# Optimization experiments

Hardware: AMD Instinct MI355X
Metric: run time of the kernel (lower is better)

## Reference

```python
import jax, jax.numpy as jnp
import numpy as np

N = 50000      # nodes
E = 800000     # edges
CIN = 128
CH = 128
COUT = 64
EPS = 1e-5     # BatchNorm eps


def setup_inputs() -> dict:
    key = jax.random.key(0)
    ks = jax.random.split(key, 16)
    s = 0.1  # weight scale for numerical stability
    return {
        "x": jax.random.normal(ks[0], (N, CIN), jnp.float32),
        "edge_index": jax.random.randint(ks[1], (2, E), 0, N, jnp.int32),
        "edge_weights": jax.random.uniform(ks[2], (E,), jnp.float32),
        "w1": jax.random.normal(ks[3], (CIN, CH), jnp.float32) * s,
        "b1": jnp.zeros((CH,), jnp.float32),
        "bn1_g": jnp.ones((CH,), jnp.float32),
        "bn1_b": jnp.zeros((CH,), jnp.float32),
        "bn1_m": jax.random.normal(ks[4], (CH,), jnp.float32) * 0.1,
        "bn1_v": jax.random.uniform(ks[5], (CH,), jnp.float32) + 0.5,
        "conv_ws": jax.random.normal(ks[6], (2, CH, CH), jnp.float32) * s,
        "conv_bs": jnp.zeros((2, CH), jnp.float32),
        "bns_g": jnp.ones((2, CH), jnp.float32),
        "bns_b": jnp.zeros((2, CH), jnp.float32),
        "bns_m": jax.random.normal(ks[7], (2, CH), jnp.float32) * 0.1,
        "bns_v": jax.random.uniform(ks[8], (2, CH), jnp.float32) + 0.5,
        "lin1_w": jax.random.normal(ks[9], (CH, CH), jnp.float32) * s,
        "lin1_b": jnp.zeros((CH,), jnp.float32),
        "lin2_w": jax.random.normal(ks[10], (CH, COUT), jnp.float32) * s,
        "lin2_b": jnp.zeros((COUT,), jnp.float32),
    }


def _bn(h, g, b, m, v):
    # BatchNorm1d in eval mode: running statistics
    return (h - m) * jax.lax.rsqrt(v + EPS) * g + b


def _gcn(h, w, b, src, dst, norm, n):
    # GCNConv: out[dst] += norm_e * (h @ W)[src]  (self loops already in src/dst)
    h = h @ w
    msg = h[src] * norm[:, None]                 # [E+N, CH]
    return jax.ops.segment_sum(msg, dst, num_segments=n) + b


def reference(x, edge_index, edge_weights, w1, b1, bn1_g, bn1_b, bn1_m, bn1_v,
              conv_ws, conv_bs, bns_g, bns_b, bns_m, bns_v,
              lin1_w, lin1_b, lin2_w, lin2_b):
    n = x.shape[0]
    loop = jnp.arange(n, dtype=edge_index.dtype)
    src = jnp.concatenate([edge_index[0], loop])
    dst = jnp.concatenate([edge_index[1], loop])
    ew = jnp.concatenate([edge_weights, jnp.ones((n,), edge_weights.dtype)])
    # symmetric degree normalization (PyG gcn_norm)
    deg = jax.ops.segment_sum(ew, dst, num_segments=n)
    dis = jnp.where(deg > 0, jax.lax.rsqrt(deg), 0.0)
    norm = dis[src] * ew * dis[dst]

    lrelu = jax.nn.leaky_relu  # slope 0.01, matches F.leaky_relu default
    h = lrelu(_bn(_gcn(x, w1, b1, src, dst, norm, n), bn1_g, bn1_b, bn1_m, bn1_v))
    for i in range(conv_ws.shape[0]):
        h = lrelu(_bn(_gcn(h, conv_ws[i], conv_bs[i], src, dst, norm, n),
                      bns_g[i], bns_b[i], bns_m[i], bns_v[i]) + h)
    h = lrelu(h @ lin1_w + lin1_b)
    # dropout is identity in eval mode
    return h @ lin2_w + lin2_b
```

## Files before the change

kernel.cpp:

```cpp
#include <hip/hip_runtime.h>
#include <hip/hip_bf16.h>


constexpr int   NN    = 50000;
constexpr int   EE    = 800000;
constexpr int   CH    = 128;
constexpr int   SLOTS = 64;
constexpr int   NBUK  = 782;
constexpr int   RCAP  = 2048;
constexpr int   EPB   = 4096;
constexpr float EPS   = 1e-5f;

typedef __attribute__((ext_vector_type(8))) short bf16x8;
typedef __attribute__((ext_vector_type(4))) float f32x4;
typedef unsigned long long u64;
typedef unsigned short u16;

__device__ inline u16 f2bf_rne(float f) {
  unsigned u = __float_as_uint(f);
  unsigned r = u + 0x7fffu + ((u >> 16) & 1u);
  return (u16)(r >> 16);
}
__device__ inline float bf2f(unsigned h16) {
  return __uint_as_float(h16 << 16);
}


__global__ __launch_bounds__(256) void bin_kernel(const int* __restrict__ ei,
                                                  const float* __restrict__ ew,
                                                  unsigned* __restrict__ gcur,
                                                  u64* __restrict__ bins) {
  __shared__ unsigned cnt[NBUK];
  __shared__ unsigned base[NBUK];
  const int tid = threadIdx.x;
  for (int b = tid; b < NBUK; b += 256) cnt[b] = 0;
  __syncthreads();
  const int e0 = blockIdx.x * EPB;
  unsigned pk[16]; u16 bkt[16]; u16 rnk[16]; unsigned char dl[16];
  #pragma unroll
  for (int i = 0; i < 16; i++) {
    int e = e0 + i * 256 + tid;
    if (e < EE) {
      int s = ei[e], d = ei[EE + e];
      float w = ew[e];
      bkt[i] = (u16)(d >> 6);
      dl[i]  = (unsigned char)(d & 63);
      pk[i]  = ((unsigned)f2bf_rne(w) << 16) | (unsigned)s;
      rnk[i] = (u16)atomicAdd(&cnt[bkt[i]], 1u);
    } else bkt[i] = 0xffffu;
  }
  __syncthreads();
  for (int b = tid; b < NBUK; b += 256) {
    unsigned c = cnt[b];
    base[b] = c ? atomicAdd(&gcur[b * 16], c) : 0u;
  }
  __syncthreads();
  #pragma unroll
  for (int i = 0; i < 16; i++) {
    if (bkt[i] == 0xffffu) continue;
    unsigned pos = base[bkt[i]] + rnk[i];
    if (pos < RCAP)
      bins[(size_t)bkt[i] * RCAP + pos] = ((u64)dl[i] << 32) | pk[i];
  }
}


__global__ __launch_bounds__(256) void scatter_kernel(const unsigned* __restrict__ gcur,
                                                      const u64* __restrict__ bins,
                                                      unsigned* __restrict__ ell,
                                                      float* __restrict__ dis) {
  __shared__ unsigned rank[64];
  __shared__ float    wsum[64];
  const int b   = blockIdx.x;
  const int tid = threadIdx.x;
  if (tid < 64) { rank[tid] = 1u; wsum[tid] = 0.f; }
  __syncthreads();
  unsigned cnt = gcur[b * 16];
  if (cnt > RCAP) cnt = RCAP;
  const u64* src = bins + (size_t)b * RCAP;
  for (unsigned i = tid; i < cnt; i += 256) {
    u64 v = src[i];
    unsigned pk = (unsigned)v;
    unsigned dl = (unsigned)(v >> 32);
    unsigned r = atomicAdd(&rank[dl], 1u);
    if (r < SLOTS)
      ell[((size_t)(b * 64 + dl)) * SLOTS + r] = pk;
    atomicAdd(&wsum[dl], bf2f(pk >> 16));
  }
  __syncthreads();
  if (tid < 64) {
    int node = b * 64 + tid;
    if (node < NN) {
      unsigned c = rank[tid];
      if (c > SLOTS) c = SLOTS;
      ell[(size_t)node * SLOTS] = c;
      dis[node] = rsqrtf(1.0f + wsum[tid]);
    }
  }
}

constexpr int NB_WZ = (73728 + 384 + 255) / 256;

__global__ void wswz_kernel(
    const float* __restrict__ w1, const float* __restrict__ bn1_g, const float* __restrict__ bn1_v,
    const float* __restrict__ conv_ws, const float* __restrict__ bns_g, const float* __restrict__ bns_v,
    const float* __restrict__ lin1_w, const float* __restrict__ lin2_w,
    const float* __restrict__ b1, const float* __restrict__ bn1_b, const float* __restrict__ bn1_m,
    const float* __restrict__ conv_bs, const float* __restrict__ bns_b, const float* __restrict__ bns_m,
    u16* __restrict__ w1h, u16* __restrict__ w1l,
    u16* __restrict__ c0h, u16* __restrict__ c0l,
    u16* __restrict__ c1h, u16* __restrict__ c1l,
    u16* __restrict__ l1h, u16* __restrict__ l1l,
    u16* __restrict__ l2h, u16* __restrict__ l2l,
    float* __restrict__ beff)
{
  int idx = blockIdx.x * 256 + threadIdx.x;
  if (idx >= 73728) {
    int r = idx - 73728;
    if (r >= 384) return;
    int l = r >> 7, c = r & 127;
    float bc, gg, bb, mm, vv;
    if (l == 0) { bc = b1[c]; gg = bn1_g[c]; bb = bn1_b[c]; mm = bn1_m[c]; vv = bn1_v[c]; }
    else {
      int o = (l - 1) * 128 + c;
      bc = conv_bs[o]; gg = bns_g[o]; bb = bns_b[o]; mm = bns_m[o]; vv = bns_v[o];
    }
    beff[r] = (bc - mm) * gg * rsqrtf(vv + EPS) + bb;
    return;
  }
  const float* W; const float* g = nullptr; const float* v = nullptr;
  u16 *hi, *lo; int CO = 128; int local;
  if      (idx < 16384) { W = w1;              g = bn1_g;     v = bn1_v;     hi = w1h; lo = w1l; local = idx; }
  else if (idx < 32768) { W = conv_ws;         g = bns_g;     v = bns_v;     hi = c0h; lo = c0l; local = idx - 16384; }
  else if (idx < 49152) { W = conv_ws + 16384; g = bns_g+128; v = bns_v+128; hi = c1h; lo = c1l; local = idx - 32768; }
  else if (idx < 65536) { W = lin1_w;                                        hi = l1h; lo = l1l; local = idx - 49152; }
  else                  { W = lin2_w;                                        hi = l2h; lo = l2l; local = idx - 65536; CO = 64; }
  int k = local / CO, n = local % CO;
  float w = W[local];
  if (g) w *= g[n] * rsqrtf(v[n] + EPS);
  int NCT = CO / 16;
  int kchunk = k >> 5, kin = k & 31, quad = kin >> 3, j = kin & 7;
  int ct = n >> 4, l = (quad << 4) | (n & 15);
  size_t pos = ((size_t)(kchunk * NCT + ct) * 64 + l) * 8 + j;
  u16 h = f2bf_rne(w);
  hi[pos] = h;
  lo[pos] = f2bf_rne(w - bf2f(h));
}

__global__ __launch_bounds__(256) void gemm1_kernel(
    const float* __restrict__ Ain,
    const u16* __restrict__ Whi, const u16* __restrict__ Wlo,
    const float* __restrict__ dis, u16* __restrict__ Cout)
{
  __shared__ float lds[64][CH + 4];
  const int tid  = threadIdx.x;
  const int wave = tid >> 6;
  const int lane = tid & 63;
  const int quad = lane >> 4;
  const int mrow = lane & 15;
  const int row0 = blockIdx.x * 64;

  int arow = row0 + wave * 16 + mrow;
  if (arow >= NN) arow = NN - 1;

  bf16x8 ahi[4], alo[4];
  const float* Ar = Ain + (size_t)arow * CH;
  #pragma unroll
  for (int c = 0; c < 4; c++) {
    int off = c * 32 + quad * 8;
    float4 f0 = *(const float4*)(Ar + off);
    float4 f1 = *(const float4*)(Ar + off + 4);
    float f[8] = {f0.x, f0.y, f0.z, f0.w, f1.x, f1.y, f1.z, f1.w};
    #pragma unroll
    for (int j = 0; j < 8; j++) {
      u16 h = f2bf_rne(f[j]);
      ahi[c][j] = (short)h;
      alo[c][j] = (short)f2bf_rne(f[j] - bf2f(h));
    }
  }

  f32x4 acc[8];
  #pragma unroll
  for (int t = 0; t < 8; t++) acc[t] = (f32x4){0.f, 0.f, 0.f, 0.f};
  #pragma unroll
  for (int c = 0; c < 4; c++) {
    #pragma unroll
    for (int t = 0; t < 8; t++) {
      size_t base = ((size_t)(c * 8 + t) * 64 + lane) * 8;
      bf16x8 bh = *(const bf16x8*)(Whi + base);
      bf16x8 bl = *(const bf16x8*)(Wlo + base);
      acc[t] = __builtin_amdgcn_mfma_f32_16x16x32_bf16(ahi[c], bh, acc[t], 0, 0, 0);
      acc[t] = __builtin_amdgcn_mfma_f32_16x16x32_bf16(alo[c], bh, acc[t], 0, 0, 0);
      acc[t] = __builtin_amdgcn_mfma_f32_16x16x32_bf16(ahi[c], bl, acc[t], 0, 0, 0);
    }
  }

  #pragma unroll
  for (int t = 0; t < 8; t++)
    #pragma unroll
    for (int r = 0; r < 4; r++)
      lds[wave * 16 + quad * 4 + r][t * 16 + mrow] = acc[t][r];
  __syncthreads();

  #pragma unroll
  for (int i = tid; i < 64 * CH / 4; i += 256) {
    int row = (i * 4) / CH;
    int col = (i * 4) % CH;
    int grow = row0 + row;
    if (grow >= NN) continue;
    float rs = dis[grow];
    const float* lp = &lds[row][col];
    u16* cp = (u16*)Cout + (size_t)grow * CH + col;
    unsigned p0 = ((unsigned)f2bf_rne(lp[1] * rs) << 16) | f2bf_rne(lp[0] * rs);
    unsigned p1 = ((unsigned)f2bf_rne(lp[3] * rs) << 16) | f2bf_rne(lp[2] * rs);
    *(uint2*)cp = make_uint2(p0, p1);
  }
}

template<bool RES>
__global__ __launch_bounds__(256, 5) void fuse_kernel(
    const u16* __restrict__ hwin,
    const unsigned* __restrict__ ell, const float* __restrict__ dis,
    const float* __restrict__ beff, const u16* __restrict__ res,
    const u16* __restrict__ Whi, const u16* __restrict__ Wlo,
    u16* __restrict__ hout, u16* __restrict__ hwout)
{
  __shared__ unsigned hs[64][68];
  const int tid  = threadIdx.x;
  const int wave = tid >> 6;
  const int lane = tid & 63;
  const int sub  = lane & 15;
  const int grp  = lane >> 4;
  const int row0 = blockIdx.x * 64;

  for (int r = 0; r < 16; r++) {
    int node = row0 + wave * 16 + r;
    int nd = node < NN ? node : NN - 1;
    unsigned myword = ell[(size_t)nd * SLOTS + lane];
    int cnt = __shfl((int)myword, 0);
    if (cnt > SLOTS) cnt = SLOTS;
    float a[8] = {0.f, 0.f, 0.f, 0.f, 0.f, 0.f, 0.f, 0.f};
    for (int j = 0; j < cnt; j += 16) {
      unsigned sidx[4]; float wv[4];
      #pragma unroll
      for (int q = 0; q < 4; q++) {
        int jj = j + q * 4 + grp;
        unsigned e = (unsigned)__shfl((int)myword, jj & 63);
        float    w = (jj == 0) ? 1.0f : bf2f(e >> 16);
        unsigned s = (jj == 0) ? (unsigned)nd : (e & 0xffffu);
        if (jj >= cnt) { w = 0.f; s = (unsigned)nd; }
        sidx[q] = s; wv[q] = w;
      }
      uint4 h[4];
      #pragma unroll
      for (int q = 0; q < 4; q++)
        h[q] = *(const uint4*)(hwin + (size_t)sidx[q] * CH + sub * 8);
      #pragma unroll
      for (int q = 0; q < 4; q++) {
        float w = wv[q];
        a[0] = fmaf(w, bf2f(h[q].x & 0xffffu), a[0]); a[1] = fmaf(w, bf2f(h[q].x >> 16), a[1]);
        a[2] = fmaf(w, bf2f(h[q].y & 0xffffu), a[2]); a[3] = fmaf(w, bf2f(h[q].y >> 16), a[3]);
        a[4] = fmaf(w, bf2f(h[q].z & 0xffffu), a[4]); a[5] = fmaf(w, bf2f(h[q].z >> 16), a[5]);
        a[6] = fmaf(w, bf2f(h[q].w & 0xffffu), a[6]); a[7] = fmaf(w, bf2f(h[q].w >> 16), a[7]);
      }
    }
    #pragma unroll
    for (int k = 0; k < 8; k++) {
      a[k] += __shfl_xor(a[k], 16);
      a[k] += __shfl_xor(a[k], 32);
    }
    if (grp == 0) {
      float disd = dis[nd];
      int c = sub * 8;
      float4 be0 = *(const float4*)(beff + c);
      float4 be1 = *(const float4*)(beff + c + 4);
      float y[8];
      y[0] = a[0] * disd + be0.x; y[1] = a[1] * disd + be0.y;
      y[2] = a[2] * disd + be0.z; y[3] = a[3] * disd + be0.w;
      y[4] = a[4] * disd + be1.x; y[5] = a[5] * disd + be1.y;
      y[6] = a[6] * disd + be1.z; y[7] = a[7] * disd + be1.w;
      if constexpr (RES) {
        uint4 rr = *(const uint4*)(res + (size_t)nd * CH + c);
        y[0] += bf2f(rr.x & 0xffffu); y[1] += bf2f(rr.x >> 16);
        y[2] += bf2f(rr.y & 0xffffu); y[3] += bf2f(rr.y >> 16);
        y[4] += bf2f(rr.z & 0xffffu); y[5] += bf2f(rr.z >> 16);
        y[6] += bf2f(rr.w & 0xffffu); y[7] += bf2f(rr.w >> 16);
      }
      #pragma unroll
      for (int k = 0; k < 8; k++) y[k] = y[k] > 0.f ? y[k] : 0.01f * y[k];
      uint4 o;
      o.x = ((unsigned)f2bf_rne(y[1]) << 16) | f2bf_rne(y[0]);
      o.y = ((unsigned)f2bf_rne(y[3]) << 16) | f2bf_rne(y[2]);
      o.z = ((unsigned)f2bf_rne(y[5]) << 16) | f2bf_rne(y[4]);
      o.w = ((unsigned)f2bf_rne(y[7]) << 16) | f2bf_rne(y[6]);
      if (node < NN) *(uint4*)(hout + (size_t)node * CH + c) = o;
      *(uint4*)&hs[wave * 16 + r][sub * 4] = o;
    }
  }

  bf16x8 af[4];
  #pragma unroll
  for (int c = 0; c < 4; c++)
    af[c] = *(const bf16x8*)&hs[wave * 16 + sub][c * 16 + grp * 4];

  f32x4 acc[8];
  #pragma unroll
  for (int t = 0; t < 8; t++) acc[t] = (f32x4){0.f, 0.f, 0.f, 0.f};
  #pragma unroll
  for (int c = 0; c < 4; c++) {
    #pragma unroll
    for (int t = 0; t < 8; t++) {
      size_t base = ((size_t)(c * 8 + t) * 64 + lane) * 8;
      bf16x8 bh = *(const bf16x8*)(Whi + base);
      bf16x8 bl = *(const bf16x8*)(Wlo + base);
      acc[t] = __builtin_amdgcn_mfma_f32_16x16x32_bf16(af[c], bh, acc[t], 0, 0, 0);
      acc[t] = __builtin_amdgcn_mfma_f32_16x16x32_bf16(af[c], bl, acc[t], 0, 0, 0);
    }
  }

  #pragma unroll
  for (int r = 0; r < 4; r++) {
    int grow = row0 + wave * 16 + grp * 4 + r;
    if (grow >= NN) continue;
    float rs = dis[grow];
    #pragma unroll
    for (int t = 0; t < 8; t++)
      hwout[(size_t)grow * CH + t * 16 + sub] = f2bf_rne(acc[t][r] * rs);
  }
}

__global__ __launch_bounds__(256, 4) void fuse_last_kernel(
    const u16* __restrict__ hwin,
    const unsigned* __restrict__ ell, const float* __restrict__ dis,
    const float* __restrict__ beff, const u16* __restrict__ res,
    const u16* __restrict__ l1h, const u16* __restrict__ l1l,
    const float* __restrict__ b1,
    const u16* __restrict__ l2h, const u16* __restrict__ l2l,
    const float* __restrict__ b2, float* __restrict__ out)
{
  __shared__ unsigned smem[64 * 132];
  float* fs = (float*)smem;
  const int tid  = threadIdx.x;
  const int wave = tid >> 6;
  const int lane = tid & 63;
  const int sub  = lane & 15;
  const int grp  = lane >> 4;
  const int row0 = blockIdx.x * 64;

  for (int r = 0; r < 16; r++) {
    int node = row0 + wave * 16 + r;
    int nd = node < NN ? node : NN - 1;
    unsigned myword = ell[(size_t)nd * SLOTS + lane];
    int cnt = __shfl((int)myword, 0);
    if (cnt > SLOTS) cnt = SLOTS;
    float a[8] = {0.f, 0.f, 0.f, 0.f, 0.f, 0.f, 0.f, 0.f};
    for (int j = 0; j < cnt; j += 16) {
      unsigned sidx[4]; float wv[4];
      #pragma unroll
      for (int q = 0; q < 4; q++) {
        int jj = j + q * 4 + grp;
        unsigned e = (unsigned)__shfl((int)myword, jj & 63);
        float    w = (jj == 0) ? 1.0f : bf2f(e >> 16);
        unsigned s = (jj == 0) ? (unsigned)nd : (e & 0xffffu);
        if (jj >= cnt) { w = 0.f; s = (unsigned)nd; }
        sidx[q] = s; wv[q] = w;
      }
      uint4 h[4];
      #pragma unroll
      for (int q = 0; q < 4; q++)
        h[q] = *(const uint4*)(hwin + (size_t)sidx[q] * CH + sub * 8);
      #pragma unroll
      for (int q = 0; q < 4; q++) {
        float w = wv[q];
        a[0] = fmaf(w, bf2f(h[q].x & 0xffffu), a[0]); a[1] = fmaf(w, bf2f(h[q].x >> 16), a[1]);
        a[2] = fmaf(w, bf2f(h[q].y & 0xffffu), a[2]); a[3] = fmaf(w, bf2f(h[q].y >> 16), a[3]);
        a[4] = fmaf(w, bf2f(h[q].z & 0xffffu), a[4]); a[5] = fmaf(w, bf2f(h[q].z >> 16), a[5]);
        a[6] = fmaf(w, bf2f(h[q].w & 0xffffu), a[6]); a[7] = fmaf(w, bf2f(h[q].w >> 16), a[7]);
      }
    }
    #pragma unroll
    for (int k = 0; k < 8; k++) {
      a[k] += __shfl_xor(a[k], 16);
      a[k] += __shfl_xor(a[k], 32);
    }
    if (grp == 0) {
      float disd = dis[nd];
      int c = sub * 8;
      float4 be0 = *(const float4*)(beff + c);
      float4 be1 = *(const float4*)(beff + c + 4);
      float y[8];
      y[0] = a[0] * disd + be0.x; y[1] = a[1] * disd + be0.y;
      y[2] = a[2] * disd + be0.z; y[3] = a[3] * disd + be0.w;
      y[4] = a[4] * disd + be1.x; y[5] = a[5] * disd + be1.y;
      y[6] = a[6] * disd + be1.z; y[7] = a[7] * disd + be1.w;
      uint4 rr = *(const uint4*)(res + (size_t)nd * CH + c);
      y[0] += bf2f(rr.x & 0xffffu); y[1] += bf2f(rr.x >> 16);
      y[2] += bf2f(rr.y & 0xffffu); y[3] += bf2f(rr.y >> 16);
      y[4] += bf2f(rr.z & 0xffffu); y[5] += bf2f(rr.z >> 16);
      y[6] += bf2f(rr.w & 0xffffu); y[7] += bf2f(rr.w >> 16);
      #pragma unroll
      for (int k = 0; k < 8; k++) y[k] = y[k] > 0.f ? y[k] : 0.01f * y[k];
      uint4 o;
      o.x = ((unsigned)f2bf_rne(y[1]) << 16) | f2bf_rne(y[0]);
      o.y = ((unsigned)f2bf_rne(y[3]) << 16) | f2bf_rne(y[2]);
      o.z = ((unsigned)f2bf_rne(y[5]) << 16) | f2bf_rne(y[4]);
      o.w = ((unsigned)f2bf_rne(y[7]) << 16) | f2bf_rne(y[6]);
      *(uint4*)&smem[(wave * 16 + r) * 68 + sub * 4] = o;
    }
  }

  bf16x8 af[4];
  #pragma unroll
  for (int c = 0; c < 4; c++)
    af[c] = *(const bf16x8*)&smem[(wave * 16 + sub) * 68 + c * 16 + grp * 4];
  __syncthreads();

  f32x4 acc[8];
  #pragma unroll
  for (int t = 0; t < 8; t++) acc[t] = (f32x4){0.f, 0.f, 0.f, 0.f};
  #pragma unroll
  for (int c = 0; c < 4; c++) {
    #pragma unroll
    for (int t = 0; t < 8; t++) {
      size_t base = ((size_t)(c * 8 + t) * 64 + lane) * 8;
      bf16x8 bh = *(const bf16x8*)(l1h + base);
      bf16x8 bl = *(const bf16x8*)(l1l + base);
      acc[t] = __builtin_amdgcn_mfma_f32_16x16x32_bf16(af[c], bh, acc[t], 0, 0, 0);
      acc[t] = __builtin_amdgcn_mfma_f32_16x16x32_bf16(af[c], bl, acc[t], 0, 0, 0);
    }
  }
  #pragma unroll
  for (int t = 0; t < 8; t++) {
    float bb = b1[t * 16 + sub];
    #pragma unroll
    for (int r = 0; r < 4; r++) {
      float x = acc[t][r] + bb;
      x = x > 0.f ? x : 0.01f * x;
      fs[(wave * 16 + grp * 4 + r) * 132 + t * 16 + sub] = x;
    }
  }

  f32x4 acc2[4];
  #pragma unroll
  for (int t = 0; t < 4; t++) acc2[t] = (f32x4){0.f, 0.f, 0.f, 0.f};
  #pragma unroll
  for (int c = 0; c < 4; c++) {
    bf16x8 ahi, alo;
    const float* lp = &fs[(wave * 16 + sub) * 132 + c * 32 + grp * 8];
    float4 f0 = *(const float4*)lp;
    float4 f1 = *(const float4*)(lp + 4);
    float f[8] = {f0.x, f0.y, f0.z, f0.w, f1.x, f1.y, f1.z, f1.w};
    #pragma unroll
    for (int j = 0; j < 8; j++) {
      u16 h = f2bf_rne(f[j]);
      ahi[j] = (short)h;
      alo[j] = (short)f2bf_rne(f[j] - bf2f(h));
    }
    #pragma unroll
    for (int t = 0; t < 4; t++) {
      size_t base = ((size_t)(c * 4 + t) * 64 + lane) * 8;
      bf16x8 bh = *(const bf16x8*)(l2h + base);
      bf16x8 bl = *(const bf16x8*)(l2l + base);
      acc2[t] = __builtin_amdgcn_mfma_f32_16x16x32_bf16(ahi, bh, acc2[t], 0, 0, 0);
      acc2[t] = __builtin_amdgcn_mfma_f32_16x16x32_bf16(alo, bh, acc2[t], 0, 0, 0);
      acc2[t] = __builtin_amdgcn_mfma_f32_16x16x32_bf16(ahi, bl, acc2[t], 0, 0, 0);
    }
  }
  #pragma unroll
  for (int t = 0; t < 4; t++) {
    float bb = b2[t * 16 + sub];
    #pragma unroll
    for (int r = 0; r < 4; r++) {
      int grow = row0 + wave * 16 + grp * 4 + r;
      if (grow < NN)
        out[(size_t)grow * 64 + t * 16 + sub] = acc2[t][r] + bb;
    }
  }
}


extern "C" void kernel_launch(void* const* d_in, const int* in_sizes, int n_in,
                              void* d_out, int out_size, void* d_ws, size_t ws_size,
                              hipStream_t stream) {
  const float* x       = (const float*)d_in[0];
  const int*   ei      = (const int*)  d_in[1];
  const float* ew      = (const float*)d_in[2];
  const float* w1      = (const float*)d_in[3];
  const float* b1      = (const float*)d_in[4];
  const float* bn1_g   = (const float*)d_in[5];
  const float* bn1_b   = (const float*)d_in[6];
  const float* bn1_m   = (const float*)d_in[7];
  const float* bn1_v   = (const float*)d_in[8];
  const float* conv_ws = (const float*)d_in[9];
  const float* conv_bs = (const float*)d_in[10];
  const float* bns_g   = (const float*)d_in[11];
  const float* bns_b   = (const float*)d_in[12];
  const float* bns_m   = (const float*)d_in[13];
  const float* bns_v   = (const float*)d_in[14];
  const float* lin1_w  = (const float*)d_in[15];
  const float* lin1_b  = (const float*)d_in[16];
  const float* lin2_w  = (const float*)d_in[17];
  const float* lin2_b  = (const float*)d_in[18];
  float* out = (float*)d_out;

  size_t off = 0;
  auto alloc = [&](size_t elems) -> void* {
    void* p = (char*)d_ws + off * 4;
    off += (elems + 3) & ~(size_t)3;
    return p;
  };
  unsigned* gcur = (unsigned*)alloc(NBUK * 16);
  u64*      bins = (u64*)     alloc((size_t)NBUK * RCAP * 2);
  unsigned* ell  = (unsigned*)alloc((size_t)NN * SLOTS);
  float*    dis  = (float*)   alloc(NN);
  float*    beff = (float*)   alloc(3 * CH);
  u16*      hwa  = (u16*)     alloc((size_t)NN * CH / 2);
  u16*      hwb  = (u16*)     alloc((size_t)NN * CH / 2);
  u16*      h1   = (u16*)     alloc((size_t)NN * CH / 2);
  u16*      h2   = (u16*)     alloc((size_t)NN * CH / 2);
  u16* w1h = (u16*)alloc(CH * CH / 2); u16* w1l = (u16*)alloc(CH * CH / 2);
  u16* c0h = (u16*)alloc(CH * CH / 2); u16* c0l = (u16*)alloc(CH * CH / 2);
  u16* c1h = (u16*)alloc(CH * CH / 2); u16* c1l = (u16*)alloc(CH * CH / 2);
  u16* l1h = (u16*)alloc(CH * CH / 2); u16* l1l = (u16*)alloc(CH * CH / 2);
  u16* l2h = (u16*)alloc(CH * 64 / 2); u16* l2l = (u16*)alloc(CH * 64 / 2);

  const int nb_bin  = (EE + EPB - 1) / EPB;
  const int nb_gemm = (NN + 63) / 64;
  dim3 B(256);

  hipMemsetAsync(gcur, 0, NBUK * 16 * sizeof(unsigned), stream);
  bin_kernel    <<<nb_bin, B, 0, stream>>>(ei, ew, gcur, bins);
  scatter_kernel<<<NBUK,   B, 0, stream>>>(gcur, bins, ell, dis);

  wswz_kernel<<<NB_WZ, B, 0, stream>>>(w1, bn1_g, bn1_v, conv_ws, bns_g, bns_v,
      lin1_w, lin2_w, b1, bn1_b, bn1_m, conv_bs, bns_b, bns_m,
      w1h, w1l, c0h, c0l, c1h, c1l, l1h, l1l, l2h, l2l, beff);

  gemm1_kernel<<<nb_gemm, B, 0, stream>>>(x, w1h, w1l, dis, hwa);

  fuse_kernel<false><<<nb_gemm, B, 0, stream>>>(hwa, ell, dis, beff, nullptr,
      c0h, c0l, h1, hwb);

  fuse_kernel<true><<<nb_gemm, B, 0, stream>>>(hwb, ell, dis, beff + CH, h1,
      c1h, c1l, h2, hwa);

  fuse_last_kernel<<<nb_gemm, B, 0, stream>>>(hwa, ell, dis, beff + 2 * CH, h2,
      l1h, l1l, lin1_b, l2h, l2l, lin2_b, out);
}
```

Measured before the change: 313.8 us.

## Shrink fused GCN blocks to 16 nodes and split GEMM columns across waves

The fused aggregate+GEMM kernels now process 16 nodes per block instead of 64. Each wave gathers 4 nodes, and the ELL row for the next node is prefetched one step ahead. The block then synchronises and each wave computes a 32-column slice (or 16 for the last layer) of the 16-row MFMA GEMM. This launches about four times as many blocks and raises the occupancy hint, aiming to improve load balance and latency hiding in the gather. The cost is an added block barrier and each block re-reading the weights for only 16 rows.

```diff
diff --git a/kernel.cpp b/kernel.cpp
--- a/kernel.cpp
+++ b/kernel.cpp
@@ -218,99 +218,109 @@
 }
 
 template<bool RES>
-__global__ __launch_bounds__(256, 5) void fuse_kernel(
+__global__ __launch_bounds__(256, 6) void fuse_kernel(
     const u16* __restrict__ hwin,
     const unsigned* __restrict__ ell, const float* __restrict__ dis,
     const float* __restrict__ beff, const u16* __restrict__ res,
     const u16* __restrict__ Whi, const u16* __restrict__ Wlo,
     u16* __restrict__ hout, u16* __restrict__ hwout)
 {
-  __shared__ unsigned hs[64][68];
+  __shared__ unsigned hs[16][68];
   const int tid  = threadIdx.x;
   const int wave = tid >> 6;
   const int lane = tid & 63;
   const int sub  = lane & 15;
   const int grp  = lane >> 4;
-  const int row0 = blockIdx.x * 64;
-
-  for (int r = 0; r < 16; r++) {
-    int node = row0 + wave * 16 + r;
-    int nd = node < NN ? node : NN - 1;
-    unsigned myword = ell[(size_t)nd * SLOTS + lane];
-    int cnt = __shfl((int)myword, 0);
-    if (cnt > SLOTS) cnt = SLOTS;
-    float a[8] = {0.f, 0.f, 0.f, 0.f, 0.f, 0.f, 0.f, 0.f};
-    for (int j = 0; j < cnt; j += 16) {
-      unsigned sidx[4]; float wv[4];
+  const int row0 = blockIdx.x * 16;
+
+  const int nbase = row0 + wave * 4;
+  {
+    int nd0 = nbase < NN ? nbase : NN - 1;
+    unsigned wcur = ell[(size_t)nd0 * SLOTS + lane];
+    for (int r = 0; r < 4; r++) {
+      int node = nbase + r;
+      int nd = node < NN ? node : NN - 1;
+      unsigned myword = wcur;
+      if (r < 3) {
+        int n2 = node + 1 < NN ? node + 1 : NN - 1;
+        wcur = ell[(size_t)n2 * SLOTS + lane];
+      }
+      int cnt = __shfl((int)myword, 0);
+      if (cnt > SLOTS) cnt = SLOTS;
+      float a[8] = {0.f, 0.f, 0.f, 0.f, 0.f, 0.f, 0.f, 0.f};
+      for (int j = 0; j < cnt; j += 16) {
+        unsigned sidx[4]; float wv[4];
+        #pragma unroll
+        for (int q = 0; q < 4; q++) {
+          int jj = j + q * 4 + grp;
+          unsigned e = (unsigned)__shfl((int)myword, jj & 63);
+          float    w = (jj == 0) ? 1.0f : bf2f(e >> 16);
+          unsigned s = (jj == 0) ? (unsigned)nd : (e & 0xffffu);
+          if (jj >= cnt) { w = 0.f; s = (unsigned)nd; }
+          sidx[q] = s; wv[q] = w;
+        }
+        uint4 h[4];
+        #pragma unroll
+        for (int q = 0; q < 4; q++)
+          h[q] = *(const uint4*)(hwin + (size_t)sidx[q] * CH + sub * 8);
+        #pragma unroll
+        for (int q = 0; q < 4; q++) {
+          float w = wv[q];
+          a[0] = fmaf(w, bf2f(h[q].x & 0xffffu), a[0]); a[1] = fmaf(w, bf2f(h[q].x >> 16), a[1]);
+          a[2] = fmaf(w, bf2f(h[q].y & 0xffffu), a[2]); a[3] = fmaf(w, bf2f(h[q].y >> 16), a[3]);
+          a[4] = fmaf(w, bf2f(h[q].z & 0xffffu), a[4]); a[5] = fmaf(w, bf2f(h[q].z >> 16), a[5]);
+          a[6] = fmaf(w, bf2f(h[q].w & 0xffffu), a[6]); a[7] = fmaf(w, bf2f(h[q].w >> 16), a[7]);
+        }
+      }
       #pragma unroll
-      for (int q = 0; q < 4; q++) {
-        int jj = j + q * 4 + grp;
-        unsigned e = (unsigned)__shfl((int)myword, jj & 63);
-        float    w = (jj == 0) ? 1.0f : bf2f(e >> 16);
-        unsigned s = (jj == 0) ? (unsigned)nd : (e & 0xffffu);
-        if (jj >= cnt) { w = 0.f; s = (unsigned)nd; }
-        sidx[q] = s; wv[q] = w;
-      }
-      uint4 h[4];
-      #pragma unroll
-      for (int q = 0; q < 4; q++)
-        h[q] = *(const uint4*)(hwin + (size_t)sidx[q] * CH + sub * 8);
-      #pragma unroll
-      for (int q = 0; q < 4; q++) {
-        float w = wv[q];
-        a[0] = fmaf(w, bf2f(h[q].x & 0xffffu), a[0]); a[1] = fmaf(w, bf2f(h[q].x >> 16), a[1]);
-        a[2] = fmaf(w, bf2f(h[q].y & 0xffffu), a[2]); a[3] = fmaf(w, bf2f(h[q].y >> 16), a[3]);
-        a[4] = fmaf(w, bf2f(h[q].z & 0xffffu), a[4]); a[5] = fmaf(w, bf2f(h[q].z >> 16), a[5]);
-        a[6] = fmaf(w, bf2f(h[q].w & 0xffffu), a[6]); a[7] = fmaf(w, bf2f(h[q].w >> 16), a[7]);
-      }
-    }
-    #pragma unroll
-    for (int k = 0; k < 8; k++) {
-      a[k] += __shfl_xor(a[k], 16);
-      a[k] += __shfl_xor(a[k], 32);
-    }
-    if (grp == 0) {
-      float disd = dis[nd];
-      int c = sub * 8;
-      float4 be0 = *(const float4*)(beff + c);
-      float4 be1 = *(const float4*)(beff + c + 4);
-      float y[8];
-      y[0] = a[0] * disd + be0.x; y[1] = a[1] * disd + be0.y;
-      y[2] = a[2] * disd + be0.z; y[3] = a[3] * disd + be0.w;
-      y[4] = a[4] * disd + be1.x; y[5] = a[5] * disd + be1.y;
-      y[6] = a[6] * disd + be1.z; y[7] = a[7] * disd + be1.w;
-      if constexpr (RES) {
-        uint4 rr = *(const uint4*)(res + (size_t)nd * CH + c);
-        y[0] += bf2f(rr.x & 0xffffu); y[1] += bf2f(rr.x >> 16);
-        y[2] += bf2f(rr.y & 0xffffu); y[3] += bf2f(rr.y >> 16);
-        y[4] += bf2f(rr.z & 0xffffu); y[5] += bf2f(rr.z >> 16);
-        y[6] += bf2f(rr.w & 0xffffu); y[7] += bf2f(rr.w >> 16);
-      }
-      #pragma unroll
-      for (int k = 0; k < 8; k++) y[k] = y[k] > 0.f ? y[k] : 0.01f * y[k];
-      uint4 o;
-      o.x = ((unsigned)f2bf_rne(y[1]) << 16) | f2bf_rne(y[0]);
-      o.y = ((unsigned)f2bf_rne(y[3]) << 16) | f2bf_rne(y[2]);
-      o.z = ((unsigned)f2bf_rne(y[5]) << 16) | f2bf_rne(y[4]);
-      o.w = ((unsigned)f2bf_rne(y[7]) << 16) | f2bf_rne(y[6]);
-      if (node < NN) *(uint4*)(hout + (size_t)node * CH + c) = o;
-      *(uint4*)&hs[wave * 16 + r][sub * 4] = o;
-    }
-  }
+      for (int k = 0; k < 8; k++) {
+        a[k] += __shfl_xor(a[k], 16);
+        a[k] += __shfl_xor(a[k], 32);
+      }
+      if (grp == 0) {
+        float disd = dis[nd];
+        int c = sub * 8;
+        float4 be0 = *(const float4*)(beff + c);
+        float4 be1 = *(const float4*)(beff + c + 4);
+        float y[8];
+        y[0] = a[0] * disd + be0.x; y[1] = a[1] * disd + be0.y;
+        y[2] = a[2] * disd + be0.z; y[3] = a[3] * disd + be0.w;
+        y[4] = a[4] * disd + be1.x; y[5] = a[5] * disd + be1.y;
+        y[6] = a[6] * disd + be1.z; y[7] = a[7] * disd + be1.w;
+        if constexpr (RES) {
+          uint4 rr = *(const uint4*)(res + (size_t)nd * CH + c);
+          y[0] += bf2f(rr.x & 0xffffu); y[1] += bf2f(rr.x >> 16);
+          y[2] += bf2f(rr.y & 0xffffu); y[3] += bf2f(rr.y >> 16);
+          y[4] += bf2f(rr.z & 0xffffu); y[5] += bf2f(rr.z >> 16);
+          y[6] += bf2f(rr.w & 0xffffu); y[7] += bf2f(rr.w >> 16);
+        }
+        #pragma unroll
+        for (int k = 0; k < 8; k++) y[k] = y[k] > 0.f ? y[k] : 0.01f * y[k];
+        uint4 o;
+        o.x = ((unsigned)f2bf_rne(y[1]) << 16) | f2bf_rne(y[0]);
+        o.y = ((unsigned)f2bf_rne(y[3]) << 16) | f2bf_rne(y[2]);
+        o.z = ((unsigned)f2bf_rne(y[5]) << 16) | f2bf_rne(y[4]);
+        o.w = ((unsigned)f2bf_rne(y[7]) << 16) | f2bf_rne(y[6]);
+        if (node < NN) *(uint4*)(hout + (size_t)node * CH + c) = o;
+        *(uint4*)&hs[wave * 4 + r][sub * 4] = o;
+      }
+    }
+  }
+  __syncthreads();
 
   bf16x8 af[4];
   #pragma unroll
   for (int c = 0; c < 4; c++)
-    af[c] = *(const bf16x8*)&hs[wave * 16 + sub][c * 16 + grp * 4];
-
-  f32x4 acc[8];
-  #pragma unroll
-  for (int t = 0; t < 8; t++) acc[t] = (f32x4){0.f, 0.f, 0.f, 0.f};
+    af[c] = *(const bf16x8*)&hs[sub][c * 16 + grp * 4];
+
+  f32x4 acc[2];
+  #pragma unroll
+  for (int t = 0; t < 2; t++) acc[t] = (f32x4){0.f, 0.f, 0.f, 0.f};
   #pragma unroll
   for (int c = 0; c < 4; c++) {
     #pragma unroll
-    for (int t = 0; t < 8; t++) {
-      size_t base = ((size_t)(c * 8 + t) * 64 + lane) * 8;
+    for (int t = 0; t < 2; t++) {
+      size_t base = ((size_t)(c * 8 + wave * 2 + t) * 64 + lane) * 8;
       bf16x8 bh = *(const bf16x8*)(Whi + base);
       bf16x8 bl = *(const bf16x8*)(Wlo + base);
       acc[t] = __builtin_amdgcn_mfma_f32_16x16x32_bf16(af[c], bh, acc[t], 0, 0, 0);
@@ -320,16 +330,16 @@
 
   #pragma unroll
   for (int r = 0; r < 4; r++) {
-    int grow = row0 + wave * 16 + grp * 4 + r;
+    int grow = row0 + grp * 4 + r;
     if (grow >= NN) continue;
     float rs = dis[grow];
     #pragma unroll
-    for (int t = 0; t < 8; t++)
-      hwout[(size_t)grow * CH + t * 16 + sub] = f2bf_rne(acc[t][r] * rs);
-  }
-}
-
-__global__ __launch_bounds__(256, 4) void fuse_last_kernel(
+    for (int t = 0; t < 2; t++)
+      hwout[(size_t)grow * CH + wave * 32 + t * 16 + sub] = f2bf_rne(acc[t][r] * rs);
+  }
+}
+
+__global__ __launch_bounds__(256, 6) void fuse_last_kernel(
     const u16* __restrict__ hwin,
     const unsigned* __restrict__ ell, const float* __restrict__ dis,
     const float* __restrict__ beff, const u16* __restrict__ res,
@@ -338,91 +348,100 @@
     const u16* __restrict__ l2h, const u16* __restrict__ l2l,
     const float* __restrict__ b2, float* __restrict__ out)
 {
-  __shared__ unsigned smem[64 * 132];
-  float* fs = (float*)smem;
+  __shared__ unsigned hs[16][68];
+  __shared__ float    fs[16][132];
   const int tid  = threadIdx.x;
   const int wave = tid >> 6;
   const int lane = tid & 63;
   const int sub  = lane & 15;
   const int grp  = lane >> 4;
-  const int row0 = blockIdx.x * 64;
-
-  for (int r = 0; r < 16; r++) {
-    int node = row0 + wave * 16 + r;
-    int nd = node < NN ? node : NN - 1;
-    unsigned myword = ell[(size_t)nd * SLOTS + lane];
-    int cnt = __shfl((int)myword, 0);
-    if (cnt > SLOTS) cnt = SLOTS;
-    float a[8] = {0.f, 0.f, 0.f, 0.f, 0.f, 0.f, 0.f, 0.f};
-    for (int j = 0; j < cnt; j += 16) {
-      unsigned sidx[4]; float wv[4];
+  const int row0 = blockIdx.x * 16;
+
+  const int nbase = row0 + wave * 4;
+  {
+    int nd0 = nbase < NN ? nbase : NN - 1;
+    unsigned wcur = ell[(size_t)nd0 * SLOTS + lane];
+    for (int r = 0; r < 4; r++) {
+      int node = nbase + r;
+      int nd = node < NN ? node : NN - 1;
+      unsigned myword = wcur;
+      if (r < 3) {
+        int n2 = node + 1 < NN ? node + 1 : NN - 1;
+        wcur = ell[(size_t)n2 * SLOTS + lane];
+      }
+      int cnt = __shfl((int)myword, 0);
+      if (cnt > SLOTS) cnt = SLOTS;
+      float a[8] = {0.f, 0.f, 0.f, 0.f, 0.f, 0.f, 0.f, 0.f};
+      for (int j = 0; j < cnt; j += 16) {
+        unsigned sidx[4]; float wv[4];
+        #pragma unroll
+        for (int q = 0; q < 4; q++) {
+          int jj = j + q * 4 + grp;
+          unsigned e = (unsigned)__shfl((int)myword, jj & 63);
+          float    w = (jj == 0) ? 1.0f : bf2f(e >> 16);
+          unsigned s = (jj == 0) ? (unsigned)nd : (e & 0xffffu);
+          if (jj >= cnt) { w = 0.f; s = (unsigned)nd; }
+          sidx[q] = s; wv[q] = w;
+        }
+        uint4 h[4];
+        #pragma unroll
+        for (int q = 0; q < 4; q++)
+          h[q] = *(const uint4*)(hwin + (size_t)sidx[q] * CH + sub * 8);
+        #pragma unroll
+        for (int q = 0; q < 4; q++) {
+          float w = wv[q];
+          a[0] = fmaf(w, bf2f(h[q].x & 0xffffu), a[0]); a[1] = fmaf(w, bf2f(h[q].x >> 16), a[1]);
+          a[2] = fmaf(w, bf2f(h[q].y & 0xffffu), a[2]); a[3] = fmaf(w, bf2f(h[q].y >> 16), a[3]);
+          a[4] = fmaf(w, bf2f(h[q].z & 0xffffu), a[4]); a[5] = fmaf(w, bf2f(h[q].z >> 16), a[5]);
+          a[6] = fmaf(w, bf2f(h[q].w & 0xffffu), a[6]); a[7] = fmaf(w, bf2f(h[q].w >> 16), a[7]);
+        }
+      }
       #pragma unroll
-      for (int q = 0; q < 4; q++) {
-        int jj = j + q * 4 + grp;
-        unsigned e = (unsigned)__shfl((int)myword, jj & 63);
-        float    w = (jj == 0) ? 1.0f : bf2f(e >> 16);
-        unsigned s = (jj == 0) ? (unsigned)nd : (e & 0xffffu);
-        if (jj >= cnt) { w = 0.f; s = (unsigned)nd; }
-        sidx[q] = s; wv[q] = w;
-      }
-      uint4 h[4];
-      #pragma unroll
-      for (int q = 0; q < 4; q++)
-        h[q] = *(const uint4*)(hwin + (size_t)sidx[q] * CH + sub * 8);
-      #pragma unroll
-      for (int q = 0; q < 4; q++) {
-        float w = wv[q];
-        a[0] = fmaf(w, bf2f(h[q].x & 0xffffu), a[0]); a[1] = fmaf(w, bf2f(h[q].x >> 16), a[1]);
-        a[2] = fmaf(w, bf2f(h[q].y & 0xffffu), a[2]); a[3] = fmaf(w, bf2f(h[q].y >> 16), a[3]);
-        a[4] = fmaf(w, bf2f(h[q].z & 0xffffu), a[4]); a[5] = fmaf(w, bf2f(h[q].z >> 16), a[5]);
-        a[6] = fmaf(w, bf2f(h[q].w & 0xffffu), a[6]); a[7] = fmaf(w, bf2f(h[q].w >> 16), a[7]);
-      }
-    }
-    #pragma unroll
-    for (int k = 0; k < 8; k++) {
-      a[k] += __shfl_xor(a[k], 16);
-      a[k] += __shfl_xor(a[k], 32);
-    }
-    if (grp == 0) {
-      float disd = dis[nd];
-      int c = sub * 8;
-      float4 be0 = *(const float4*)(beff + c);
-      float4 be1 = *(const float4*)(beff + c + 4);
-      float y[8];
-      y[0] = a[0] * disd + be0.x; y[1] = a[1] * disd + be0.y;
-      y[2] = a[2] * disd + be0.z; y[3] = a[3] * disd + be0.w;
-      y[4] = a[4] * disd + be1.x; y[5] = a[5] * disd + be1.y;
-      y[6] = a[6] * disd + be1.z; y[7] = a[7] * disd + be1.w;
-      uint4 rr = *(const uint4*)(res + (size_t)nd * CH + c);
-      y[0] += bf2f(rr.x & 0xffffu); y[1] += bf2f(rr.x >> 16);
-      y[2] += bf2f(rr.y & 0xffffu); y[3] += bf2f(rr.y >> 16);
-      y[4] += bf2f(rr.z & 0xffffu); y[5] += bf2f(rr.z >> 16);
-      y[6] += bf2f(rr.w & 0xffffu); y[7] += bf2f(rr.w >> 16);
-      #pragma unroll
-      for (int k = 0; k < 8; k++) y[k] = y[k] > 0.f ? y[k] : 0.01f * y[k];
-      uint4 o;
-      o.x = ((unsigned)f2bf_rne(y[1]) << 16) | f2bf_rne(y[0]);
-      o.y = ((unsigned)f2bf_rne(y[3]) << 16) | f2bf_rne(y[2]);
-      o.z = ((unsigned)f2bf_rne(y[5]) << 16) | f2bf_rne(y[4]);
-      o.w = ((unsigned)f2bf_rne(y[7]) << 16) | f2bf_rne(y[6]);
-      *(uint4*)&smem[(wave * 16 + r) * 68 + sub * 4] = o;
-    }
-  }
+      for (int k = 0; k < 8; k++) {
+        a[k] += __shfl_xor(a[k], 16);
+        a[k] += __shfl_xor(a[k], 32);
+      }
+      if (grp == 0) {
+        float disd = dis[nd];
+        int c = sub * 8;
+        float4 be0 = *(const float4*)(beff + c);
+        float4 be1 = *(const float4*)(beff + c + 4);
+        float y[8];
+        y[0] = a[0] * disd + be0.x; y[1] = a[1] * disd + be0.y;
+        y[2] = a[2] * disd + be0.z; y[3] = a[3] * disd + be0.w;
+        y[4] = a[4] * disd + be1.x; y[5] = a[5] * disd + be1.y;
+        y[6] = a[6] * disd + be1.z; y[7] = a[7] * disd + be1.w;
+        uint4 rr = *(const uint4*)(res + (size_t)nd * CH + c);
+        y[0] += bf2f(rr.x & 0xffffu); y[1] += bf2f(rr.x >> 16);
+        y[2] += bf2f(rr.y & 0xffffu); y[3] += bf2f(rr.y >> 16);
+        y[4] += bf2f(rr.z & 0xffffu); y[5] += bf2f(rr.z >> 16);
+        y[6] += bf2f(rr.w & 0xffffu); y[7] += bf2f(rr.w >> 16);
+        #pragma unroll
+        for (int k = 0; k < 8; k++) y[k] = y[k] > 0.f ? y[k] : 0.01f * y[k];
+        uint4 o;
+        o.x = ((unsigned)f2bf_rne(y[1]) << 16) | f2bf_rne(y[0]);
+        o.y = ((unsigned)f2bf_rne(y[3]) << 16) | f2bf_rne(y[2]);
+        o.z = ((unsigned)f2bf_rne(y[5]) << 16) | f2bf_rne(y[4]);
+        o.w = ((unsigned)f2bf_rne(y[7]) << 16) | f2bf_rne(y[6]);
+        *(uint4*)&hs[wave * 4 + r][sub * 4] = o;
+      }
+    }
+  }
+  __syncthreads();
 
   bf16x8 af[4];
   #pragma unroll
   for (int c = 0; c < 4; c++)
-    af[c] = *(const bf16x8*)&smem[(wave * 16 + sub) * 68 + c * 16 + grp * 4];
-  __syncthreads();
-
-  f32x4 acc[8];
-  #pragma unroll
-  for (int t = 0; t < 8; t++) acc[t] = (f32x4){0.f, 0.f, 0.f, 0.f};
+    af[c] = *(const bf16x8*)&hs[sub][c * 16 + grp * 4];
+
+  f32x4 acc[2];
+  #pragma unroll
+  for (int t = 0; t < 2; t++) acc[t] = (f32x4){0.f, 0.f, 0.f, 0.f};
   #pragma unroll
   for (int c = 0; c < 4; c++) {
     #pragma unroll
-    for (int t = 0; t < 8; t++) {
-      size_t base = ((size_t)(c * 8 + t) * 64 + lane) * 8;
+    for (int t = 0; t < 2; t++) {
+      size_t base = ((size_t)(c * 8 + wave * 2 + t) * 64 + lane) * 8;
       bf16x8 bh = *(const bf16x8*)(l1h + base);
       bf16x8 bl = *(const bf16x8*)(l1l + base);
       acc[t] = __builtin_amdgcn_mfma_f32_16x16x32_bf16(af[c], bh, acc[t], 0, 0, 0);
@@ -430,23 +449,23 @@
     }
   }
   #pragma unroll
-  for (int t = 0; t < 8; t++) {
-    float bb = b1[t * 16 + sub];
+  for (int t = 0; t < 2; t++) {
+    int col = wave * 32 + t * 16 + sub;
+    float bb = b1[col];
     #pragma unroll
     for (int r = 0; r < 4; r++) {
       float x = acc[t][r] + bb;
       x = x > 0.f ? x : 0.01f * x;
-      fs[(wave * 16 + grp * 4 + r) * 132 + t * 16 + sub] = x;
-    }
-  }
-
-  f32x4 acc2[4];
-  #pragma unroll
-  for (int t = 0; t < 4; t++) acc2[t] = (f32x4){0.f, 0.f, 0.f, 0.f};
+      fs[grp * 4 + r][col] = x;
+    }
+  }
+  __syncthreads();
+
+  f32x4 acc2 = (f32x4){0.f, 0.f, 0.f, 0.f};
   #pragma unroll
   for (int c = 0; c < 4; c++) {
     bf16x8 ahi, alo;
-    const float* lp = &fs[(wave * 16 + sub) * 132 + c * 32 + grp * 8];
+    const float* lp = &fs[sub][c * 32 + grp * 8];
     float4 f0 = *(const float4*)lp;
     float4 f1 = *(const float4*)(lp + 4);
     float f[8] = {f0.x, f0.y, f0.z, f0.w, f1.x, f1.y, f1.z, f1.w};
@@ -456,24 +475,20 @@
       ahi[j] = (short)h;
       alo[j] = (short)f2bf_rne(f[j] - bf2f(h));
     }
-    #pragma unroll
-    for (int t = 0; t < 4; t++) {
-      size_t base = ((size_t)(c * 4 + t) * 64 + lane) * 8;
-      bf16x8 bh = *(const bf16x8*)(l2h + base);
-      bf16x8 bl = *(const bf16x8*)(l2l + base);
-      acc2[t] = __builtin_amdgcn_mfma_f32_16x16x32_bf16(ahi, bh, acc2[t], 0, 0, 0);
-      acc2[t] = __builtin_amdgcn_mfma_f32_16x16x32_bf16(alo, bh, acc2[t], 0, 0, 0);
-      acc2[t] = __builtin_amdgcn_mfma_f32_16x16x32_bf16(ahi, bl, acc2[t], 0, 0, 0);
-    }
-  }
-  #pragma unroll
-  for (int t = 0; t < 4; t++) {
-    float bb = b2[t * 16 + sub];
+    size_t base = ((size_t)(c * 4 + wave) * 64 + lane) * 8;
+    bf16x8 bh = *(const bf16x8*)(l2h + base);
+    bf16x8 bl = *(const bf16x8*)(l2l + base);
+    acc2 = __builtin_amdgcn_mfma_f32_16x16x32_bf16(ahi, bh, acc2, 0, 0, 0);
+    acc2 = __builtin_amdgcn_mfma_f32_16x16x32_bf16(alo, bh, acc2, 0, 0, 0);
+    acc2 = __builtin_amdgcn_mfma_f32_16x16x32_bf16(ahi, bl, acc2, 0, 0, 0);
+  }
+  {
+    float bb = b2[wave * 16 + sub];
     #pragma unroll
     for (int r = 0; r < 4; r++) {
-      int grow = row0 + wave * 16 + grp * 4 + r;
+      int grow = row0 + grp * 4 + r;
       if (grow < NN)
-        out[(size_t)grow * 64 + t * 16 + sub] = acc2[t][r] + bb;
+        out[(size_t)grow * 64 + wave * 16 + sub] = acc2[r] + bb;
     }
   }
 }
@@ -526,6 +541,7 @@
 
   const int nb_bin  = (EE + EPB - 1) / EPB;
   const int nb_gemm = (NN + 63) / 64;
+  const int nb_fuse = (NN + 15) / 16;
   dim3 B(256);
 
   hipMemsetAsync(gcur, 0, NBUK * 16 * sizeof(unsigned), stream);
@@ -538,12 +554,12 @@
 
   gemm1_kernel<<<nb_gemm, B, 0, stream>>>(x, w1h, w1l, dis, hwa);
 
-  fuse_kernel<false><<<nb_gemm, B, 0, stream>>>(hwa, ell, dis, beff, nullptr,
+  fuse_kernel<false><<<nb_fuse, B, 0, stream>>>(hwa, ell, dis, beff, nullptr,
       c0h, c0l, h1, hwb);
 
-  fuse_kernel<true><<<nb_gemm, B, 0, stream>>>(hwb, ell, dis, beff + CH, h1,
+  fuse_kernel<true><<<nb_fuse, B, 0, stream>>>(hwb, ell, dis, beff + CH, h1,
       c1h, c1l, h2, hwa);
 
-  fuse_last_kernel<<<nb_gemm, B, 0, stream>>>(hwa, ell, dis, beff + 2 * CH, h2,
+  fuse_last_kernel<<<nb_fuse, B, 0, stream>>>(hwa, ell, dis, beff + 2 * CH, h2,
       l1h, l1l, lin1_b, l2h, l2l, lin2_b, out);
 }
```

After: 298.5 us. -4.9%, faster.
